# Kernel optimization log

Hardware: AMD Instinct MI355X
Metric: run time of the kernel (lower is better)

Reference implementation:

```python
import jax, jax.numpy as jnp
import numpy as np

N_HEADS = 16
D_MODEL = 1024
D_K = D_MODEL // N_HEADS
B, S = 2, 2048


def setup_inputs() -> dict:
    key = jax.random.key(0)
    ks = jax.random.split(key, 12)
    sc = 1.0 / np.sqrt(D_MODEL)
    inp = {
        'query': jax.random.normal(ks[0], (B, S, D_MODEL), jnp.float32),
        'key':   jax.random.normal(ks[1], (B, S, D_MODEL), jnp.float32),
        'value': jax.random.normal(ks[2], (B, S, D_MODEL), jnp.float32),
        'mask':  jnp.ones((B, 1, 1, S), jnp.int32),
        'Wq': jax.random.normal(ks[3], (D_MODEL, D_MODEL), jnp.float32) * sc,
        'bq': jnp.zeros((D_MODEL,), jnp.float32),
        'Wk': jax.random.normal(ks[4], (D_MODEL, D_MODEL), jnp.float32) * sc,
        'bk': jnp.zeros((D_MODEL,), jnp.float32),
        'Wv': jax.random.normal(ks[5], (D_MODEL, D_MODEL), jnp.float32) * sc,
        'bv': jnp.zeros((D_MODEL,), jnp.float32),
        'Wo': jax.random.normal(ks[6], (D_MODEL, D_MODEL), jnp.float32) * sc,
        'bo': jnp.zeros((D_MODEL,), jnp.float32),
    }
    return inp


def reference(query, key, value, mask, Wq, bq, Wk, bk, Wv, bv, Wo, bo):
    # Linear projections (torch Linear: x @ W.T + b)
    q = query @ Wq.T + bq
    k = key @ Wk.T + bk
    v = value @ Wv.T + bv
    # [B, S, D] -> [B, H, S, d_k]
    def split_heads(x):
        b, s, _ = x.shape
        return x.reshape(b, s, N_HEADS, D_K).transpose(0, 2, 1, 3)
    q, k, v = split_heads(q), split_heads(k), split_heads(v)
    # scaled dot-product attention with explicit [B,H,S,S] scores
    att = jnp.einsum('bhqd,bhkd->bhqk', q, k) / jnp.sqrt(jnp.float32(D_K))
    att = jnp.where(mask == 0, -jnp.inf, att)
    scores = jax.nn.softmax(att, axis=-1)
    # dropout is identity in eval/reference mode
    out = jnp.einsum('bhqk,bhkd->bhqd', scores, v)
    b = out.shape[0]
    out = out.transpose(0, 2, 1, 3).reshape(b, -1, N_HEADS * D_K)
    return out @ Wo.T + bo
```

## Files before the change

### kernel.cpp

```cpp
#include <hip/hip_runtime.h>
#include <hip/hip_bf16.h>

#define DM   1024
#define SLEN 2048
#define NH   16
#define DK   64

typedef float f32x4 __attribute__((ext_vector_type(4)));
typedef short short8 __attribute__((ext_vector_type(8)));

__device__ __forceinline__ unsigned short f2bf(float f) {
  union { float f; unsigned int u; } x; x.f = f;
  unsigned int r = x.u + 0x7fffu + ((x.u >> 16) & 1u);
  return (unsigned short)(r >> 16);
}

__device__ __forceinline__ void gload_lds16(const unsigned short* g, unsigned short* l) {
  __builtin_amdgcn_global_load_lds(
      (const __attribute__((address_space(1))) unsigned int*)g,
      (__attribute__((address_space(3))) unsigned int*)l, 16, 0, 0);
}

struct ConvArgs { const float* src[7]; unsigned short* dst[7]; };

__global__ __launch_bounds__(256) void conv_kernel(ConvArgs a) {
  int blk = blockIdx.x, seg, base;
  if (blk < 6144) { seg = blk >> 11; base = blk & 2047; }
  else { int t = blk - 6144; seg = 3 + (t >> 9); base = t & 511; }
  const float* s = a.src[seg];
  unsigned short* d = a.dst[seg];
  int idx = (base * 256 + (int)threadIdx.x) * 8;
  float4 v0 = *(const float4*)(s + idx);
  float4 v1 = *(const float4*)(s + idx + 4);
  unsigned short o[8];
  o[0]=f2bf(v0.x); o[1]=f2bf(v0.y); o[2]=f2bf(v0.z); o[3]=f2bf(v0.w);
  o[4]=f2bf(v1.x); o[5]=f2bf(v1.y); o[6]=f2bf(v1.z); o[7]=f2bf(v1.w);
  *(uint4*)(d + idx) = *(uint4*)o;
}

template <int TN>
__device__ __forceinline__ void gemm_core(int mode,
                                          const unsigned short* __restrict__ A,
                                          const unsigned short* __restrict__ W,
                                          const float* __restrict__ bias,
                                          void* __restrict__ outp, float scale,
                                          int m0, int n0,
                                          unsigned short* As, unsigned short* Bs) {
  const int tid = threadIdx.x;
  const int lane = tid & 63;
  const int wv = tid >> 6;
  const int wm = (wv >> 1) * 64, wn = (wv & 1) * (TN / 2);
  const int NB = TN / 32;

  f32x4 acc[4][NB];
#pragma unroll
  for (int i = 0; i < 4; ++i)
#pragma unroll
    for (int j = 0; j < NB; ++j) acc[i][j] = (f32x4){0.f, 0.f, 0.f, 0.f};

  for (int k0 = 0; k0 < DM; k0 += 32) {
    __syncthreads();
#pragma unroll
    for (int i = 0; i < 2; ++i) {
      int c = tid + i * 256;
      gload_lds16(A + (size_t)(m0 + (c >> 2)) * DM + k0 + ((c & 3) << 3), As + c * 8);
    }
#pragma unroll
    for (int i = 0; i < TN / 64; ++i) {
      int c = tid + i * 256;
      gload_lds16(W + (size_t)(n0 + (c >> 2)) * DM + k0 + ((c & 3) << 3), Bs + c * 8);
    }
    __syncthreads();
    short8 af[4], bf[NB];
#pragma unroll
    for (int i = 0; i < 4; ++i)
      af[i] = *(const short8*)(As + (wm + i * 16 + (lane & 15)) * 32 + ((lane >> 4) << 3));
#pragma unroll
    for (int j = 0; j < NB; ++j)
      bf[j] = *(const short8*)(Bs + (wn + j * 16 + (lane & 15)) * 32 + ((lane >> 4) << 3));
#pragma unroll
    for (int i = 0; i < 4; ++i)
#pragma unroll
      for (int j = 0; j < NB; ++j)
        acc[i][j] = __builtin_amdgcn_mfma_f32_16x16x32_bf16(af[i], bf[j], acc[i][j], 0, 0, 0);
  }

#pragma unroll
  for (int i = 0; i < 4; ++i)
#pragma unroll
    for (int j = 0; j < NB; ++j) {
      int col = n0 + wn + j * 16 + (lane & 15);
      float bv = bias[col];
      int row0 = wm + i * 16 + ((lane >> 4) << 2) + m0;
      if (mode == 2) {
        unsigned short pk[4];
#pragma unroll
        for (int g = 0; g < 4; ++g) pk[g] = f2bf(acc[i][j][g] + bv);
        int d = col & (DK - 1), hh = col >> 6;
        int brow = row0 >> 11, srow = row0 & (SLEN - 1);
        size_t idx = ((size_t)((brow * NH + hh) * DK + d)) * SLEN + srow;
        *(uint2*)(((unsigned short*)outp) + idx) = *(uint2*)pk;
      } else if (mode == 0) {
#pragma unroll
        for (int g = 0; g < 4; ++g) {
          int row = row0 + g;
          float v = (acc[i][j][g] + bv) * scale;
          size_t idx = ((size_t)((row >> 11) * NH + (col >> 6))) * (SLEN * DK) +
                       (size_t)(row & (SLEN - 1)) * DK + (col & (DK - 1));
          ((unsigned short*)outp)[idx] = f2bf(v);
        }
      } else {
#pragma unroll
        for (int g = 0; g < 4; ++g)
          ((float*)outp)[(size_t)(row0 + g) * DM + col] = acc[i][j][g] + bv;
      }
    }
}

struct QKVArgs {
  const unsigned short* A[3];
  const unsigned short* W[3];
  const float* bias[3];
  unsigned short* out[3];
  float scale[3];
  int mode[3];
};

__global__ __launch_bounds__(256) void gemm_qkv_kernel(QKVArgs a) {
  __shared__ unsigned short As[128 * 32], Bs[128 * 32];
  int z = blockIdx.z;
  gemm_core<128>(a.mode[z], a.A[z], a.W[z], a.bias[z], a.out[z], a.scale[z],
                 blockIdx.x * 128, blockIdx.y * 128, As, Bs);
}

__global__ __launch_bounds__(256) void gemm_o_kernel(const unsigned short* __restrict__ A,
                                                     const unsigned short* __restrict__ W,
                                                     const float* __restrict__ bias,
                                                     float* __restrict__ out) {
  __shared__ unsigned short As[128 * 32], Bs[64 * 32];
  gemm_core<64>(1, A, W, bias, out, 1.0f, blockIdx.x * 128, blockIdx.y * 64, As, Bs);
}

__global__ __launch_bounds__(512) void attn_kernel(
    const unsigned short* __restrict__ Qw,
    const unsigned short* __restrict__ Kw,
    const unsigned short* __restrict__ Vtw,
    const int* __restrict__ mask,
    unsigned short* __restrict__ attn_out) {
  __shared__ unsigned short QPs[128 * 72];
  __shared__ unsigned short Ks[64 * 72];
  __shared__ unsigned short Vts[64 * 72];
  __shared__ float maskadd[64];

  const int tid = threadIdx.x;
  const int lane = tid & 63;
  const int wv = tid >> 6;
  const int s0 = blockIdx.x * 128;
  const int bh = blockIdx.y;
  const int b = bh >> 4, h = bh & 15;
  const unsigned short* Qb = Qw + (size_t)bh * (SLEN * DK);
  const unsigned short* Kb = Kw + (size_t)bh * (SLEN * DK);
  const unsigned short* Vtb = Vtw + (size_t)bh * (SLEN * DK);

#pragma unroll
  for (int i = 0; i < 2; ++i) {
    int seg = tid + i * 512;
    int row = seg >> 3, d0 = (seg & 7) << 3;
    *(uint4*)(QPs + row * 72 + d0) = *(const uint4*)(Qb + (size_t)(s0 + row) * DK + d0);
  }

  const int srow = tid >> 3, scol = (tid & 7) << 3;
  uint4 kreg = *(const uint4*)(Kb + (size_t)srow * DK + scol);
  uint4 vreg = *(const uint4*)(Vtb + (size_t)srow * SLEN + scol);
  int mreg = (tid < 64) ? mask[b * SLEN + tid] : 1;

  __syncthreads();
  const int qb = wv * 16;
  short8 aq[2];
#pragma unroll
  for (int ks = 0; ks < 2; ++ks)
    aq[ks] = *(const short8*)(QPs + (qb + (lane & 15)) * 72 + ks * 32 + ((lane >> 4) << 3));

  float lsum[4] = {0.f, 0.f, 0.f, 0.f};
  f32x4 O[4];
#pragma unroll
  for (int dt = 0; dt < 4; ++dt) O[dt] = (f32x4){0.f, 0.f, 0.f, 0.f};

  for (int kt = 0; kt < SLEN / 64; ++kt) {
    if (kt) __syncthreads();
    *(uint4*)(Ks + srow * 72 + scol) = kreg;
    *(uint4*)(Vts + srow * 72 + scol) = vreg;
    if (tid < 64) maskadd[tid] = mreg ? 0.0f : -1e30f;
    __syncthreads();
    if (kt < SLEN / 64 - 1) {
      const int kv1 = (kt + 1) * 64;
      kreg = *(const uint4*)(Kb + (size_t)(kv1 + srow) * DK + scol);
      vreg = *(const uint4*)(Vtb + (size_t)srow * SLEN + kv1 + scol);
      if (tid < 64) mreg = mask[b * SLEN + kv1 + tid];
    }

    f32x4 sc[4];
#pragma unroll
    for (int c = 0; c < 4; ++c) {
      short8 bk0 = *(const short8*)(Ks + (c * 16 + (lane & 15)) * 72 + ((lane >> 4) << 3));
      short8 bk1 = *(const short8*)(Ks + (c * 16 + (lane & 15)) * 72 + 32 + ((lane >> 4) << 3));
      f32x4 z = (f32x4){0.f, 0.f, 0.f, 0.f};
      z = __builtin_amdgcn_mfma_f32_16x16x32_bf16(aq[0], bk0, z, 0, 0, 0);
      sc[c] = __builtin_amdgcn_mfma_f32_16x16x32_bf16(aq[1], bk1, z, 0, 0, 0);
    }

    __hip_bfloat16* Pp = (__hip_bfloat16*)QPs;
    const int row0 = qb + ((lane >> 4) << 2);
#pragma unroll
    for (int c = 0; c < 4; ++c) {
      int colp = c * 16 + (lane & 15);
      float ma = maskadd[colp];
      float p0 = __builtin_exp2f(sc[c][0] + ma);
      float p1 = __builtin_exp2f(sc[c][1] + ma);
      float p2 = __builtin_exp2f(sc[c][2] + ma);
      float p3 = __builtin_exp2f(sc[c][3] + ma);
      lsum[0] += p0; lsum[1] += p1; lsum[2] += p2; lsum[3] += p3;
      __hip_bfloat162 h01 = __float22bfloat162_rn(float2{p0, p1});
      __hip_bfloat162 h23 = __float22bfloat162_rn(float2{p2, p3});
      Pp[(row0 + 0) * 72 + colp] = h01.x;
      Pp[(row0 + 1) * 72 + colp] = h01.y;
      Pp[(row0 + 2) * 72 + colp] = h23.x;
      Pp[(row0 + 3) * 72 + colp] = h23.y;
    }

    short8 ap[2];
#pragma unroll
    for (int ks = 0; ks < 2; ++ks)
      ap[ks] = *(const short8*)(QPs + (qb + (lane & 15)) * 72 + ks * 32 + ((lane >> 4) << 3));
#pragma unroll
    for (int dt = 0; dt < 4; ++dt) {
      short8 bv0 = *(const short8*)(Vts + (dt * 16 + (lane & 15)) * 72 + ((lane >> 4) << 3));
      short8 bv1 = *(const short8*)(Vts + (dt * 16 + (lane & 15)) * 72 + 32 + ((lane >> 4) << 3));
      O[dt] = __builtin_amdgcn_mfma_f32_16x16x32_bf16(ap[0], bv0, O[dt], 0, 0, 0);
      O[dt] = __builtin_amdgcn_mfma_f32_16x16x32_bf16(ap[1], bv1, O[dt], 0, 0, 0);
    }
  }

#pragma unroll
  for (int g = 0; g < 4; ++g) {
    float rs = lsum[g];
    rs += __shfl_xor(rs, 1);
    rs += __shfl_xor(rs, 2);
    rs += __shfl_xor(rs, 4);
    rs += __shfl_xor(rs, 8);
    float inv = 1.0f / rs;
    int row = s0 + qb + ((lane >> 4) << 2) + g;
#pragma unroll
    for (int dt = 0; dt < 4; ++dt) {
      int col = h * DK + dt * 16 + (lane & 15);
      attn_out[(size_t)(b * SLEN + row) * DM + col] = f2bf(O[dt][g] * inv);
    }
  }
}

extern "C" void kernel_launch(void* const* d_in, const int* in_sizes, int n_in,
                              void* d_out, int out_size, void* d_ws, size_t ws_size,
                              hipStream_t stream) {
  (void)in_sizes; (void)n_in; (void)out_size; (void)ws_size;
  const float* query = (const float*)d_in[0];
  const float* key_  = (const float*)d_in[1];
  const float* value = (const float*)d_in[2];
  const int*   mask  = (const int*)d_in[3];
  const float* Wq = (const float*)d_in[4];
  const float* bq = (const float*)d_in[5];
  const float* Wk = (const float*)d_in[6];
  const float* bk = (const float*)d_in[7];
  const float* Wv = (const float*)d_in[8];
  const float* bv = (const float*)d_in[9];
  const float* Wo = (const float*)d_in[10];
  const float* bo = (const float*)d_in[11];
  float* out = (float*)d_out;

  const size_t WSZ = 1048576, XSZ = 4194304;
  unsigned short* base = (unsigned short*)d_ws;
  unsigned short* Wqb = base;
  unsigned short* Wkb = base + WSZ;
  unsigned short* Wvb = base + 2 * WSZ;
  unsigned short* Wob = base + 3 * WSZ;
  unsigned short* Xqb = base + 4 * WSZ;
  unsigned short* Xkb = Xqb + XSZ;
  unsigned short* Xvb = Xqb + 2 * XSZ;
  unsigned short* Qw  = Xqb + 3 * XSZ;
  unsigned short* Kw  = Qw + XSZ;
  unsigned short* Vtw = Qw + 2 * XSZ;
  unsigned short* attnb = Qw + 3 * XSZ;

  ConvArgs ca;
  ca.src[0] = query; ca.src[1] = key_; ca.src[2] = value;
  ca.src[3] = Wq; ca.src[4] = Wk; ca.src[5] = Wv; ca.src[6] = Wo;
  ca.dst[0] = Xqb; ca.dst[1] = Xkb; ca.dst[2] = Xvb;
  ca.dst[3] = Wqb; ca.dst[4] = Wkb; ca.dst[5] = Wvb; ca.dst[6] = Wob;
  conv_kernel<<<8192, 256, 0, stream>>>(ca);

  QKVArgs qa;
  qa.A[0] = Xqb; qa.A[1] = Xkb; qa.A[2] = Xvb;
  qa.W[0] = Wqb; qa.W[1] = Wkb; qa.W[2] = Wvb;
  qa.bias[0] = bq; qa.bias[1] = bk; qa.bias[2] = bv;
  qa.out[0] = Qw; qa.out[1] = Kw; qa.out[2] = Vtw;
  qa.scale[0] = 0.18033688011112042f;
  qa.scale[1] = 1.0f; qa.scale[2] = 1.0f;
  qa.mode[0] = 0; qa.mode[1] = 0; qa.mode[2] = 2;
  gemm_qkv_kernel<<<dim3(32, 8, 3), 256, 0, stream>>>(qa);

  attn_kernel<<<dim3(16, 32), 512, 0, stream>>>(Qw, Kw, Vtw, mask, attnb);

  gemm_o_kernel<<<dim3(32, 16), 256, 0, stream>>>(attnb, Wob, bo, out);
}
```

Measured before the change: 256.6 us.

## Split attention KV loop across wave groups and swizzle GEMM LDS with K=64 tiles

The GEMM core now stages 64-wide K tiles with an XOR-swizzled LDS layout, halving the barrier count and avoiding bank conflicts. The attention kernel is restructured: two wave groups each process alternate KV tiles with async global-to-LDS loads. Each wave handles 32 query rows using transposed S^T so P stays in registers and feeds 16x16x16 MFMAs directly, dropping the LDS round-trip for P. Partial O and row sums are merged through LDS at the end. This adds LDS usage and a final reduction step, and raises register pressure under a launch bound of 4.

```diff
diff --git a/kernel.cpp b/kernel.cpp
--- a/kernel.cpp
+++ b/kernel.cpp
@@ -8,6 +8,7 @@
 
 typedef float f32x4 __attribute__((ext_vector_type(4)));
 typedef short short8 __attribute__((ext_vector_type(8)));
+typedef short short4v __attribute__((ext_vector_type(4)));
 
 __device__ __forceinline__ unsigned short f2bf(float f) {
   union { float f; unsigned int u; } x; x.f = f;
@@ -19,6 +20,21 @@
   __builtin_amdgcn_global_load_lds(
       (const __attribute__((address_space(1))) unsigned int*)g,
       (__attribute__((address_space(3))) unsigned int*)l, 16, 0, 0);
+}
+
+__device__ __forceinline__ f32x4 mfma32(short8 a, short8 b, f32x4 c) {
+  return __builtin_amdgcn_mfma_f32_16x16x32_bf16(a, b, c, 0, 0, 0);
+}
+
+__device__ __forceinline__ f32x4 mfma16(short4v a, short4v b, f32x4 c) {
+#if __has_builtin(__builtin_amdgcn_mfma_f32_16x16x16bf16_1k)
+  return __builtin_amdgcn_mfma_f32_16x16x16bf16_1k(a, b, c, 0, 0, 0);
+#else
+  f32x4 d;
+  asm volatile("v_mfma_f32_16x16x16_bf16 %0, %1, %2, %3"
+               : "=v"(d) : "v"(a), "v"(b), "v"(c));
+  return d;
+#endif
 }
 
 struct ConvArgs { const float* src[7]; unsigned short* dst[7]; };
@@ -48,6 +64,8 @@
                                           unsigned short* As, unsigned short* Bs) {
   const int tid = threadIdx.x;
   const int lane = tid & 63;
+  const int l15 = lane & 15;
+  const int quad = lane >> 4;
   const int wv = tid >> 6;
   const int wm = (wv >> 1) * 64, wn = (wv & 1) * (TN / 2);
   const int NB = TN / 32;
@@ -58,40 +76,52 @@
 #pragma unroll
     for (int j = 0; j < NB; ++j) acc[i][j] = (f32x4){0.f, 0.f, 0.f, 0.f};
 
-  for (int k0 = 0; k0 < DM; k0 += 32) {
+  for (int k0 = 0; k0 < DM; k0 += 64) {
     __syncthreads();
 #pragma unroll
-    for (int i = 0; i < 2; ++i) {
+    for (int i = 0; i < 4; ++i) {
       int c = tid + i * 256;
-      gload_lds16(A + (size_t)(m0 + (c >> 2)) * DM + k0 + ((c & 3) << 3), As + c * 8);
-    }
-#pragma unroll
-    for (int i = 0; i < TN / 64; ++i) {
+      int row = c >> 3, sc = ((c & 7) ^ (row & 7)) << 3;
+      gload_lds16(A + (size_t)(m0 + row) * DM + k0 + sc, As + c * 8);
+    }
+#pragma unroll
+    for (int i = 0; i < NB; ++i) {
       int c = tid + i * 256;
-      gload_lds16(W + (size_t)(n0 + (c >> 2)) * DM + k0 + ((c & 3) << 3), Bs + c * 8);
+      int row = c >> 3, sc = ((c & 7) ^ (row & 7)) << 3;
+      gload_lds16(W + (size_t)(n0 + row) * DM + k0 + sc, Bs + c * 8);
     }
     __syncthreads();
-    short8 af[4], bf[NB];
-#pragma unroll
-    for (int i = 0; i < 4; ++i)
-      af[i] = *(const short8*)(As + (wm + i * 16 + (lane & 15)) * 32 + ((lane >> 4) << 3));
-#pragma unroll
-    for (int j = 0; j < NB; ++j)
-      bf[j] = *(const short8*)(Bs + (wn + j * 16 + (lane & 15)) * 32 + ((lane >> 4) << 3));
-#pragma unroll
-    for (int i = 0; i < 4; ++i)
-#pragma unroll
-      for (int j = 0; j < NB; ++j)
-        acc[i][j] = __builtin_amdgcn_mfma_f32_16x16x32_bf16(af[i], bf[j], acc[i][j], 0, 0, 0);
+    short8 af[4][2], bf[NB][2];
+#pragma unroll
+    for (int i = 0; i < 4; ++i) {
+      int r = wm + i * 16 + l15;
+#pragma unroll
+      for (int kf = 0; kf < 2; ++kf)
+        af[i][kf] = *(const short8*)(As + r * 64 + (((kf * 4 + quad) ^ (r & 7)) << 3));
+    }
+#pragma unroll
+    for (int j = 0; j < NB; ++j) {
+      int r = wn + j * 16 + l15;
+#pragma unroll
+      for (int kf = 0; kf < 2; ++kf)
+        bf[j][kf] = *(const short8*)(Bs + r * 64 + (((kf * 4 + quad) ^ (r & 7)) << 3));
+    }
+#pragma unroll
+    for (int kf = 0; kf < 2; ++kf)
+#pragma unroll
+      for (int i = 0; i < 4; ++i)
+#pragma unroll
+        for (int j = 0; j < NB; ++j)
+          acc[i][j] = mfma32(af[i][kf], bf[j][kf], acc[i][j]);
   }
 
 #pragma unroll
   for (int i = 0; i < 4; ++i)
 #pragma unroll
     for (int j = 0; j < NB; ++j) {
-      int col = n0 + wn + j * 16 + (lane & 15);
+      int col = n0 + wn + j * 16 + l15;
       float bv = bias[col];
-      int row0 = wm + i * 16 + ((lane >> 4) << 2) + m0;
+      int row0 = wm + i * 16 + (quad << 2) + m0;
       if (mode == 2) {
         unsigned short pk[4];
 #pragma unroll
@@ -127,7 +157,7 @@
 };
 
 __global__ __launch_bounds__(256) void gemm_qkv_kernel(QKVArgs a) {
-  __shared__ unsigned short As[128 * 32], Bs[128 * 32];
+  __shared__ unsigned short As[128 * 64], Bs[128 * 64];
   int z = blockIdx.z;
   gemm_core<128>(a.mode[z], a.A[z], a.W[z], a.bias[z], a.out[z], a.scale[z],
                  blockIdx.x * 128, blockIdx.y * 128, As, Bs);
@@ -137,24 +167,35 @@
                                                      const unsigned short* __restrict__ W,
                                                      const float* __restrict__ bias,
                                                      float* __restrict__ out) {
-  __shared__ unsigned short As[128 * 32], Bs[64 * 32];
+  __shared__ unsigned short As[128 * 64], Bs[64 * 64];
   gemm_core<64>(1, A, W, bias, out, 1.0f, blockIdx.x * 128, blockIdx.y * 64, As, Bs);
 }
 
-__global__ __launch_bounds__(512) void attn_kernel(
+__global__ __launch_bounds__(512, 4) void attn_kernel(
     const unsigned short* __restrict__ Qw,
     const unsigned short* __restrict__ Kw,
     const unsigned short* __restrict__ Vtw,
     const int* __restrict__ mask,
     unsigned short* __restrict__ attn_out) {
-  __shared__ unsigned short QPs[128 * 72];
-  __shared__ unsigned short Ks[64 * 72];
-  __shared__ unsigned short Vts[64 * 72];
-  __shared__ float maskadd[64];
+  __shared__ uint4 smem4[3264];
+  char* smb = (char*)smem4;
+  unsigned short* Qs = (unsigned short*)smb;
 
   const int tid = threadIdx.x;
   const int lane = tid & 63;
+  const int l15 = lane & 15;
+  const int quad = lane >> 4;
   const int wv = tid >> 6;
+  const int grp = wv >> 2;
+  const int widx = wv & 3;
+  const int tg = tid & 255;
+
+  unsigned short* KstG = (unsigned short*)(smb + 18432 + grp * 8192);
+  unsigned short* VstG = (unsigned short*)(smb + 34816 + grp * 8192);
+  float* maskG = (float*)(smb + 51200 + grp * 256);
+  float* Oex = (float*)(smb + 18432);
+  float* lsX = (float*)(smb + 51456);
+
   const int s0 = blockIdx.x * 128;
   const int bh = blockIdx.y;
   const int b = bh >> 4, h = bh & 15;
@@ -166,94 +207,138 @@
   for (int i = 0; i < 2; ++i) {
     int seg = tid + i * 512;
     int row = seg >> 3, d0 = (seg & 7) << 3;
-    *(uint4*)(QPs + row * 72 + d0) = *(const uint4*)(Qb + (size_t)(s0 + row) * DK + d0);
-  }
-
-  const int srow = tid >> 3, scol = (tid & 7) << 3;
-  uint4 kreg = *(const uint4*)(Kb + (size_t)srow * DK + scol);
-  uint4 vreg = *(const uint4*)(Vtb + (size_t)srow * SLEN + scol);
-  int mreg = (tid < 64) ? mask[b * SLEN + tid] : 1;
-
+    *(uint4*)(Qs + row * 72 + d0) = *(const uint4*)(Qb + (size_t)(s0 + row) * DK + d0);
+  }
+
+  const int c0 = tg, c1 = tg + 256;
+  const int r0c = c0 >> 3, s0c = ((c0 & 7) ^ (r0c & 7)) << 3;
+  const int r1c = c1 >> 3, s1c = ((c1 & 7) ^ (r1c & 7)) << 3;
+
+  int kv0 = grp * 64;
+  gload_lds16(Kb + (size_t)(kv0 + r0c) * DK + s0c, KstG + c0 * 8);
+  gload_lds16(Kb + (size_t)(kv0 + r1c) * DK + s1c, KstG + c1 * 8);
+  gload_lds16(Vtb + (size_t)r0c * SLEN + kv0 + s0c, VstG + c0 * 8);
+  gload_lds16(Vtb + (size_t)r1c * SLEN + kv0 + s1c, VstG + c1 * 8);
+  int mreg = (tg < 64) ? mask[b * SLEN + kv0 + tg] : 1;
   __syncthreads();
-  const int qb = wv * 16;
-  short8 aq[2];
-#pragma unroll
-  for (int ks = 0; ks < 2; ++ks)
-    aq[ks] = *(const short8*)(QPs + (qb + (lane & 15)) * 72 + ks * 32 + ((lane >> 4) << 3));
-
-  float lsum[4] = {0.f, 0.f, 0.f, 0.f};
-  f32x4 O[4];
-#pragma unroll
-  for (int dt = 0; dt < 4; ++dt) O[dt] = (f32x4){0.f, 0.f, 0.f, 0.f};
-
-  for (int kt = 0; kt < SLEN / 64; ++kt) {
-    if (kt) __syncthreads();
-    *(uint4*)(Ks + srow * 72 + scol) = kreg;
-    *(uint4*)(Vts + srow * 72 + scol) = vreg;
-    if (tid < 64) maskadd[tid] = mreg ? 0.0f : -1e30f;
+  if (tg < 64) {
+    maskG[tg] = mreg ? 0.0f : -1e30f;
+    mreg = mask[b * SLEN + (2 + grp) * 64 + tg];
+  }
+  __syncthreads();
+
+  const int qb = widx * 32;
+  short8 bq[2][2];
+#pragma unroll
+  for (int qt = 0; qt < 2; ++qt)
+#pragma unroll
+    for (int kf = 0; kf < 2; ++kf)
+      bq[qt][kf] = *(const short8*)(Qs + (qb + qt * 16 + l15) * 72 + kf * 32 + quad * 8);
+
+  f32x4 O[4][2];
+#pragma unroll
+  for (int dt = 0; dt < 4; ++dt)
+#pragma unroll
+    for (int qt = 0; qt < 2; ++qt) O[dt][qt] = (f32x4){0.f, 0.f, 0.f, 0.f};
+  float lsum[2] = {0.f, 0.f};
+
+  for (int it = 0; it < 16; ++it) {
+    f32x4 st[4][2];
+#pragma unroll
+    for (int ct = 0; ct < 4; ++ct) {
+      int r = ct * 16 + l15;
+      short8 ka0 = *(const short8*)(KstG + r * 64 + ((quad ^ (r & 7)) << 3));
+      short8 ka1 = *(const short8*)(KstG + r * 64 + (((4 + quad) ^ (r & 7)) << 3));
+#pragma unroll
+      for (int qt = 0; qt < 2; ++qt) {
+        f32x4 z = (f32x4){0.f, 0.f, 0.f, 0.f};
+        z = mfma32(ka0, bq[qt][0], z);
+        st[ct][qt] = mfma32(ka1, bq[qt][1], z);
+      }
+    }
+    short4v pf[4][2];
+#pragma unroll
+    for (int ct = 0; ct < 4; ++ct) {
+      f32x4 ma = *(const f32x4*)(maskG + ct * 16 + quad * 4);
+#pragma unroll
+      for (int qt = 0; qt < 2; ++qt) {
+        float p0 = __builtin_exp2f(st[ct][qt][0] + ma[0]);
+        float p1 = __builtin_exp2f(st[ct][qt][1] + ma[1]);
+        float p2 = __builtin_exp2f(st[ct][qt][2] + ma[2]);
+        float p3 = __builtin_exp2f(st[ct][qt][3] + ma[3]);
+        lsum[qt] += (p0 + p1) + (p2 + p3);
+        union { short4v s; __hip_bfloat162 h[2]; } u;
+        u.h[0] = __float22bfloat162_rn(float2{p0, p1});
+        u.h[1] = __float22bfloat162_rn(float2{p2, p3});
+        pf[ct][qt] = u.s;
+      }
+    }
+#pragma unroll
+    for (int dt = 0; dt < 4; ++dt) {
+      int rd = dt * 16 + l15;
+      short4v vf[4];
+#pragma unroll
+      for (int ct = 0; ct < 4; ++ct) {
+        int slot = (ct * 2 + (quad >> 1)) ^ (rd & 7);
+        vf[ct] = *(const short4v*)(VstG + rd * 64 + slot * 8 + (quad & 1) * 4);
+      }
+#pragma unroll
+      for (int qt = 0; qt < 2; ++qt)
+#pragma unroll
+        for (int ct = 0; ct < 4; ++ct)
+          O[dt][qt] = mfma16(vf[ct], pf[ct][qt], O[dt][qt]);
+    }
     __syncthreads();
-    if (kt < SLEN / 64 - 1) {
-      const int kv1 = (kt + 1) * 64;
-      kreg = *(const uint4*)(Kb + (size_t)(kv1 + srow) * DK + scol);
-      vreg = *(const uint4*)(Vtb + (size_t)srow * SLEN + kv1 + scol);
-      if (tid < 64) mreg = mask[b * SLEN + kv1 + tid];
-    }
-
-    f32x4 sc[4];
-#pragma unroll
-    for (int c = 0; c < 4; ++c) {
-      short8 bk0 = *(const short8*)(Ks + (c * 16 + (lane & 15)) * 72 + ((lane >> 4) << 3));
-      short8 bk1 = *(const short8*)(Ks + (c * 16 + (lane & 15)) * 72 + 32 + ((lane >> 4) << 3));
-      f32x4 z = (f32x4){0.f, 0.f, 0.f, 0.f};
-      z = __builtin_amdgcn_mfma_f32_16x16x32_bf16(aq[0], bk0, z, 0, 0, 0);
-      sc[c] = __builtin_amdgcn_mfma_f32_16x16x32_bf16(aq[1], bk1, z, 0, 0, 0);
-    }
-
-    __hip_bfloat16* Pp = (__hip_bfloat16*)QPs;
-    const int row0 = qb + ((lane >> 4) << 2);
-#pragma unroll
-    for (int c = 0; c < 4; ++c) {
-      int colp = c * 16 + (lane & 15);
-      float ma = maskadd[colp];
-      float p0 = __builtin_exp2f(sc[c][0] + ma);
-      float p1 = __builtin_exp2f(sc[c][1] + ma);
-      float p2 = __builtin_exp2f(sc[c][2] + ma);
-      float p3 = __builtin_exp2f(sc[c][3] + ma);
-      lsum[0] += p0; lsum[1] += p1; lsum[2] += p2; lsum[3] += p3;
-      __hip_bfloat162 h01 = __float22bfloat162_rn(float2{p0, p1});
-      __hip_bfloat162 h23 = __float22bfloat162_rn(float2{p2, p3});
-      Pp[(row0 + 0) * 72 + colp] = h01.x;
-      Pp[(row0 + 1) * 72 + colp] = h01.y;
-      Pp[(row0 + 2) * 72 + colp] = h23.x;
-      Pp[(row0 + 3) * 72 + colp] = h23.y;
-    }
-
-    short8 ap[2];
-#pragma unroll
-    for (int ks = 0; ks < 2; ++ks)
-      ap[ks] = *(const short8*)(QPs + (qb + (lane & 15)) * 72 + ks * 32 + ((lane >> 4) << 3));
-#pragma unroll
-    for (int dt = 0; dt < 4; ++dt) {
-      short8 bv0 = *(const short8*)(Vts + (dt * 16 + (lane & 15)) * 72 + ((lane >> 4) << 3));
-      short8 bv1 = *(const short8*)(Vts + (dt * 16 + (lane & 15)) * 72 + 32 + ((lane >> 4) << 3));
-      O[dt] = __builtin_amdgcn_mfma_f32_16x16x32_bf16(ap[0], bv0, O[dt], 0, 0, 0);
-      O[dt] = __builtin_amdgcn_mfma_f32_16x16x32_bf16(ap[1], bv1, O[dt], 0, 0, 0);
-    }
-  }
-
-#pragma unroll
-  for (int g = 0; g < 4; ++g) {
-    float rs = lsum[g];
-    rs += __shfl_xor(rs, 1);
-    rs += __shfl_xor(rs, 2);
-    rs += __shfl_xor(rs, 4);
-    rs += __shfl_xor(rs, 8);
-    float inv = 1.0f / rs;
-    int row = s0 + qb + ((lane >> 4) << 2) + g;
-#pragma unroll
-    for (int dt = 0; dt < 4; ++dt) {
-      int col = h * DK + dt * 16 + (lane & 15);
-      attn_out[(size_t)(b * SLEN + row) * DM + col] = f2bf(O[dt][g] * inv);
+    if (it < 15) {
+      int kvn = ((it + 1) * 2 + grp) * 64;
+      gload_lds16(Kb + (size_t)(kvn + r0c) * DK + s0c, KstG + c0 * 8);
+      gload_lds16(Kb + (size_t)(kvn + r1c) * DK + s1c, KstG + c1 * 8);
+      gload_lds16(Vtb + (size_t)r0c * SLEN + kvn + s0c, VstG + c0 * 8);
+      gload_lds16(Vtb + (size_t)r1c * SLEN + kvn + s1c, VstG + c1 * 8);
+      if (tg < 64) {
+        maskG[tg] = mreg ? 0.0f : -1e30f;
+        if (it < 14) mreg = mask[b * SLEN + ((it + 2) * 2 + grp) * 64 + tg];
+      }
+      __syncthreads();
+    }
+  }
+
+#pragma unroll
+  for (int qt = 0; qt < 2; ++qt) {
+    lsum[qt] += __shfl_xor(lsum[qt], 16);
+    lsum[qt] += __shfl_xor(lsum[qt], 32);
+  }
+  if (grp == 1) {
+#pragma unroll
+    for (int dt = 0; dt < 4; ++dt)
+#pragma unroll
+      for (int qt = 0; qt < 2; ++qt) {
+        int qg = qb + qt * 16 + l15;
+#pragma unroll
+        for (int i = 0; i < 4; ++i)
+          Oex[(dt * 16 + quad * 4 + i) * 129 + qg] = O[dt][qt][i];
+      }
+    if (quad == 0) {
+      lsX[qb + lane] = lsum[0];
+      lsX[qb + 16 + lane] = lsum[1];
+    }
+  }
+  __syncthreads();
+  if (grp == 0) {
+#pragma unroll
+    for (int qt = 0; qt < 2; ++qt) {
+      int qg = qb + qt * 16 + l15;
+      float inv = 1.0f / (lsum[qt] + lsX[qg]);
+      int srow = s0 + qg;
+#pragma unroll
+      for (int dt = 0; dt < 4; ++dt) {
+        int d0 = dt * 16 + quad * 4;
+        unsigned short pk[4];
+#pragma unroll
+        for (int i = 0; i < 4; ++i)
+          pk[i] = f2bf((O[dt][qt][i] + Oex[(d0 + i) * 129 + qg]) * inv);
+        *(uint2*)(attn_out + (size_t)(b * SLEN + srow) * DM + h * DK + d0) = *(uint2*)pk;
+      }
     }
   }
 }
```

Result: faster. 248.4 us (-3.2%).
